# Kernel optimization log

Hardware: AMD Instinct MI355X
Metric: run time of the kernel (lower is better)

The kernel has to match this reference:

```python
import jax, jax.numpy as jnp
import numpy as np

BS, NS, NCP, NH, C, HID, R = 8, 2048, 8, 8, 128, 128, 128


def rotation_6d_to_matrix(d6):
    a1, a2 = d6[..., :3], d6[..., 3:]
    b1 = a1 / jnp.linalg.norm(a1, axis=-1, keepdims=True)
    b2 = a2 - jnp.sum(b1 * a2, axis=-1, keepdims=True) * b1
    b2 = b2 / jnp.linalg.norm(b2, axis=-1, keepdims=True)
    b3 = jnp.cross(b1, b2)
    return jnp.stack([b1, b2, b3], axis=-2)  # (..., 3, 3), rows b1,b2,b3


def _sample_plane(plane, uv):
    # plane: (B,C,R,R); uv: (B,N,2) in [0,1]; uv[...,0]->width, uv[...,1]->height
    Rr = plane.shape[-1]
    x = jnp.clip(uv[..., 0], 0.0, 1.0) * (Rr - 1)
    y = jnp.clip(uv[..., 1], 0.0, 1.0) * (Rr - 1)
    x0 = jnp.floor(x); y0 = jnp.floor(y)
    wx = x - x0; wy = y - y0
    x0i = x0.astype(jnp.int32); y0i = y0.astype(jnp.int32)
    x1i = jnp.minimum(x0i + 1, Rr - 1); y1i = jnp.minimum(y0i + 1, Rr - 1)
    gb = jax.vmap(lambda p, yi, xi: p[:, yi, xi])  # per-batch gather -> (C,N)
    f00 = gb(plane, y0i, x0i); f01 = gb(plane, y0i, x1i)
    f10 = gb(plane, y1i, x0i); f11 = gb(plane, y1i, x1i)
    wx = wx[:, None, :]; wy = wy[:, None, :]
    f = f00 * (1 - wx) * (1 - wy) + f01 * wx * (1 - wy) + f10 * (1 - wx) * wy + f11 * wx * wy
    return jnp.transpose(f, (0, 2, 1))  # (B,N,C)


def triplane_sample(p, pxz, pxy, pyz):
    # p: (B,N,3) in [0,1]^3; sum of bilinear samples from the three planes
    return (_sample_plane(pxz, p[..., jnp.array([0, 2])])
            + _sample_plane(pxy, p[..., jnp.array([0, 1])])
            + _sample_plane(pyz, p[..., jnp.array([1, 2])]))


def setup_inputs() -> dict:
    key = jax.random.key(0)
    ks = jax.random.split(key, 10)
    s = 1.0 / np.sqrt(C)
    return {
        "query_pos": jax.random.uniform(ks[0], (BS, NS, 9), dtype=jnp.float32),
        "plane_xz": jax.random.normal(ks[1], (BS, C, R, R), dtype=jnp.float32),
        "plane_xy": jax.random.normal(ks[2], (BS, C, R, R), dtype=jnp.float32),
        "plane_yz": jax.random.normal(ks[3], (BS, C, R, R), dtype=jnp.float32),
        "control_points": jax.random.normal(ks[4], (NCP, 3), dtype=jnp.float32) * 0.05,
        "W_v": jax.random.normal(ks[5], (C, HID), dtype=jnp.float32) * s,
        "b_v": jnp.zeros((HID,), jnp.float32),
        "W_w": jax.random.normal(ks[6], (C, NCP * NH), dtype=jnp.float32) * s,
        "b_w": jnp.zeros((NCP * NH,), jnp.float32),
        "W_o": jax.random.normal(ks[7], (HID, C), dtype=jnp.float32) * s,
        "b_o": jnp.zeros((C,), jnp.float32),
    }


def reference(query_pos, plane_xz, plane_xy, plane_yz, control_points,
              W_v, b_v, W_w, b_w, W_o, b_o):
    bs, ns, _ = query_pos.shape
    q_ori = query_pos[..., 3:]
    q_pos = query_pos[..., :3]
    feature = triplane_sample(q_pos, plane_xz, plane_xy, plane_yz)  # (bs,ns,C)
    rot = rotation_6d_to_matrix(q_ori)  # (bs,ns,3,3)
    # rotate control points: einsum('bnpd,bngd->bngp') with cp broadcast over (bs,ns)
    cp = jnp.einsum('bnpd,gd->bngp', rot, control_points)  # (bs,ns,ncp,3)
    anchor = q_pos[:, :, None, :] + cp  # (bs,ns,ncp,3)
    sf = triplane_sample(anchor.reshape(bs, ns * NCP, 3), plane_xz, plane_xy, plane_yz)
    sf = sf.reshape(bs * ns, NCP, C)  # head dim in torch code is a pure repeat
    feat = feature.reshape(bs * ns, C)
    w = (feat @ W_w + b_w).reshape(bs * ns, NCP, NH)  # (B,ncp,heads)
    vbase = sf @ W_v + b_v  # (B,ncp,hid); identical across repeated head dim
    # torch: (v * weights).sum((1,2)) with v_t[b,i,j,k]=vbase[b,j,k], w[b,i,j]
    out = jnp.einsum('bjk,bij->bk', vbase, w)  # (B,hid)
    out = out @ W_o + b_o
    out = out + feat
    return out.reshape(bs, ns, -1)
```

## Files before the change

### kernel.cpp

```cpp
#include <hip/hip_runtime.h>
#include <hip/hip_fp16.h>
#include <math.h>

constexpr int BS  = 8;
constexpr int NS  = 2048;
constexpr int NCP = 8;
constexpr int NH  = 8;
constexpr int C   = 128;
constexpr int HID = 128;
constexpr int RR  = 128;

constexpr int QPB = 8;
constexpr int VEC = 4;

constexpr size_t PLE = (size_t)BS * RR * RR * C;

struct F4 { float x, y, z, w; };
__device__ __forceinline__ F4 f4add(F4 a, F4 b) {
    return F4{a.x + b.x, a.y + b.y, a.z + b.z, a.w + b.w};
}
__device__ __forceinline__ F4 f4fma(F4 acc, float s, F4 v) {
    return F4{fmaf(s, v.x, acc.x), fmaf(s, v.y, acc.y),
              fmaf(s, v.z, acc.z), fmaf(s, v.w, acc.w)};
}
__device__ __forceinline__ F4 cvt4(int2 r) {
    __half2 h0 = *reinterpret_cast<__half2*>(&r.x);
    __half2 h1 = *reinterpret_cast<__half2*>(&r.y);
    float2 f0 = __half22float2(h0);
    float2 f1 = __half22float2(h1);
    return F4{f0.x, f0.y, f1.x, f1.y};
}

__global__ __launch_bounds__(256) void transpose_k(
    const float* __restrict__ pxz, const float* __restrict__ pxy,
    const float* __restrict__ pyz, __half* __restrict__ dst)
{
    const int z  = blockIdx.z;
    const int pl = z >> 3;
    const int b  = z & 7;
    const float* src = (pl == 0 ? pxz : (pl == 1 ? pxy : pyz)) + (size_t)b * C * RR * RR;
    __half* d = dst + (size_t)z * (RR * RR * C);

    __shared__ float tile[32][33];
    const int N  = RR * RR;
    const int n0 = blockIdx.x * 32;
    const int m0 = blockIdx.y * 32;
    const int tx = threadIdx.x, ty = threadIdx.y;

    #pragma unroll
    for (int ii = 0; ii < 4; ++ii)
        tile[ty + ii * 8][tx] = src[(size_t)(m0 + ty + ii * 8) * N + n0 + tx];
    __syncthreads();
    #pragma unroll
    for (int ii = 0; ii < 4; ++ii)
        d[(size_t)(n0 + ty + ii * 8) * C + m0 + tx] = __float2half(tile[tx][ty + ii * 8]);
}

__global__ __launch_bounds__(128) void prepw_k(
    const float* __restrict__ Wv, const float* __restrict__ bv,
    const float* __restrict__ Ww, const float* __restrict__ bw,
    const float* __restrict__ Wo,
    float* __restrict__ Wf, float* __restrict__ bf,
    float* __restrict__ Ww2, float* __restrict__ bw2)
{
    const int k = blockIdx.x, c = threadIdx.x;
    if (k < 128) {
        float acc = 0.f;
        #pragma unroll 8
        for (int j = 0; j < 128; ++j) acc += Wv[k * 128 + j] * Wo[j * 128 + c];
        Wf[k * 128 + c] = acc;
    } else if (k == 128) {
        float acc = 0.f;
        #pragma unroll 8
        for (int j = 0; j < 128; ++j) acc += bv[j] * Wo[j * 128 + c];
        bf[c] = acc;
    } else {
        float s[NH];
        #pragma unroll
        for (int h = 0; h < NH; ++h) s[h] = 0.f;
        #pragma unroll
        for (int i = 0; i < NCP; ++i)
            #pragma unroll
            for (int h = 0; h < NH; ++h) s[h] += Ww[c * (NCP * NH) + i * NH + h];
        #pragma unroll
        for (int h = 0; h < NH; ++h) Ww2[c * NH + h] = s[h];
        if (c < NH) {
            float t = 0.f;
            #pragma unroll
            for (int i = 0; i < NCP; ++i) t += bw[i * NH + c];
            bw2[c] = t;
        }
    }
}

__device__ __forceinline__ F4 samp(const __half* __restrict__ base, float u, float v)
{
    float x = fminf(fmaxf(u, 0.f), 1.f) * (float)(RR - 1);
    float y = fminf(fmaxf(v, 0.f), 1.f) * (float)(RR - 1);
    float x0f = floorf(x), y0f = floorf(y);
    float wx = x - x0f, wy = y - y0f;
    int x0 = (int)x0f, y0 = (int)y0f;
    int x1 = min(x0 + 1, RR - 1), y1 = min(y0 + 1, RR - 1);
    int r0 = y0 << 14, r1 = y1 << 14, cc0 = x0 << 7, cc1 = x1 << 7;
    int2 a00 = *reinterpret_cast<const int2*>(base + r0 + cc0);
    int2 a01 = *reinterpret_cast<const int2*>(base + r0 + cc1);
    int2 a10 = *reinterpret_cast<const int2*>(base + r1 + cc0);
    int2 a11 = *reinterpret_cast<const int2*>(base + r1 + cc1);
    float w00 = (1.f - wx) * (1.f - wy), w01 = wx * (1.f - wy);
    float w10 = (1.f - wx) * wy,         w11 = wx * wy;
    F4 f00 = cvt4(a00), f01 = cvt4(a01), f10 = cvt4(a10), f11 = cvt4(a11);
    F4 r;
    r.x = f00.x * w00 + f01.x * w01 + f10.x * w10 + f11.x * w11;
    r.y = f00.y * w00 + f01.y * w01 + f10.y * w10 + f11.y * w11;
    r.z = f00.z * w00 + f01.z * w01 + f10.z * w10 + f11.z * w11;
    r.w = f00.w * w00 + f01.w * w01 + f10.w * w10 + f11.w * w11;
    return r;
}

__global__ __launch_bounds__(256) void attn_k(
    const float* __restrict__ qpos,
    const __half* __restrict__ planes,
    const float* __restrict__ cpts,
    const float* __restrict__ Ww2, const float* __restrict__ bw2,
    const float* __restrict__ Wf,  const float* __restrict__ bf,
    const float* __restrict__ bo,
    float* __restrict__ out)
{
    const int nb   = gridDim.x;
    const int cpx  = nb >> 3;
    const int sbid = (blockIdx.x & 7) * cpx + (blockIdx.x >> 3);

    const int tid  = threadIdx.x;
    const int ql   = tid >> 5;
    const int lane = tid & 31;
    const int c4   = lane * VEC;
    const int q    = sbid * QPB + ql;
    const int b    = q >> 11;

    const float* qp = qpos + (size_t)q * 9;
    const float px = qp[0], py = qp[1], pz = qp[2];
    const float a1x = qp[3], a1y = qp[4], a1z = qp[5];
    const float a2x = qp[6], a2y = qp[7], a2z = qp[8];

    float inv = 1.f / sqrtf(a1x * a1x + a1y * a1y + a1z * a1z);
    float b1x = a1x * inv, b1y = a1y * inv, b1z = a1z * inv;
    float dd  = b1x * a2x + b1y * a2y + b1z * a2z;
    float b2x = a2x - dd * b1x, b2y = a2y - dd * b1y, b2z = a2z - dd * b1z;
    inv = 1.f / sqrtf(b2x * b2x + b2y * b2y + b2z * b2z);
    b2x *= inv; b2y *= inv; b2z *= inv;
    float b3x = b1y * b2z - b1z * b2y;
    float b3y = b1z * b2x - b1x * b2z;
    float b3z = b1x * b2y - b1y * b2x;

    const __half* Pxz = planes + (size_t)b * (RR * RR * C) + c4;
    const __half* Pxy = Pxz + PLE;
    const __half* Pyz = Pxy + PLE;

    F4 feat = f4add(f4add(samp(Pxz, px, pz), samp(Pxy, px, py)), samp(Pyz, py, pz));

    float p[NH];
    #pragma unroll
    for (int h = 0; h < NH; ++h) p[h] = 0.f;
    {
        const float* wr = Ww2 + c4 * NH;
        const float fv[VEC] = {feat.x, feat.y, feat.z, feat.w};
        #pragma unroll
        for (int i = 0; i < VEC; ++i)
            #pragma unroll
            for (int h = 0; h < NH; ++h) p[h] += fv[i] * wr[i * NH + h];
    }
    #pragma unroll
    for (int off = 16; off >= 1; off >>= 1)
        #pragma unroll
        for (int h = 0; h < NH; ++h) p[h] += __shfl_xor(p[h], off);

    float ws[NH], Ssum = 0.f;
    #pragma unroll
    for (int h = 0; h < NH; ++h) { ws[h] = p[h] + bw2[h]; Ssum += ws[h]; }

    F4 comb = {0.f, 0.f, 0.f, 0.f};
    #pragma unroll 2
    for (int g = 0; g < NCP; ++g) {
        float cx = cpts[g * 3 + 0], cy = cpts[g * 3 + 1], cz = cpts[g * 3 + 2];
        float ax = px + b1x * cx + b1y * cy + b1z * cz;
        float ay = py + b2x * cx + b2y * cy + b2z * cz;
        float az = pz + b3x * cx + b3y * cy + b3z * cz;
        F4 s = f4add(f4add(samp(Pxz, ax, az), samp(Pxy, ax, ay)), samp(Pyz, ay, az));
        comb = f4fma(comb, ws[g], s);
    }

    __shared__ float sComb[QPB][C];
    __shared__ float sFeat[QPB][C];
    __shared__ float sSum[QPB];
    *reinterpret_cast<float4*>(&sComb[ql][c4]) = make_float4(comb.x, comb.y, comb.z, comb.w);
    *reinterpret_cast<float4*>(&sFeat[ql][c4]) = make_float4(feat.x, feat.y, feat.z, feat.w);
    if (lane == 0) sSum[ql] = Ssum;
    __syncthreads();

    const int c  = tid & 127;
    const int q0 = (tid >> 7) * 4;
    float acc[4];
    const float bfc = bf[c], boc = bo[c];
    #pragma unroll
    for (int j = 0; j < 4; ++j)
        acc[j] = sSum[q0 + j] * bfc + boc + sFeat[q0 + j][c];
    #pragma unroll 4
    for (int k = 0; k < C; ++k) {
        float wf = Wf[k * C + c];
        #pragma unroll
        for (int j = 0; j < 4; ++j) acc[j] += sComb[q0 + j][k] * wf;
    }
    #pragma unroll
    for (int j = 0; j < 4; ++j)
        out[(size_t)(sbid * QPB + q0 + j) * C + c] = acc[j];
}

extern "C" void kernel_launch(void* const* d_in, const int* in_sizes, int n_in,
                              void* d_out, int out_size, void* d_ws, size_t ws_size,
                              hipStream_t stream)
{
    const float* qpos = (const float*)d_in[0];
    const float* pxz  = (const float*)d_in[1];
    const float* pxy  = (const float*)d_in[2];
    const float* pyz  = (const float*)d_in[3];
    const float* cpts = (const float*)d_in[4];
    const float* Wv   = (const float*)d_in[5];
    const float* bv   = (const float*)d_in[6];
    const float* Ww   = (const float*)d_in[7];
    const float* bw   = (const float*)d_in[8];
    const float* Wo   = (const float*)d_in[9];
    const float* bo   = (const float*)d_in[10];
    float* out = (float*)d_out;

    __half* plh = (__half*)d_ws;
    float*  wsf = (float*)((char*)d_ws + 3 * PLE * sizeof(__half));
    float* Wf  = wsf;
    float* bf  = Wf + C * HID;
    float* Ww2 = bf + C;
    float* bw2 = Ww2 + C * NH;

    {
        dim3 tb(32, 8, 1);
        dim3 tg(RR * RR / 32, C / 32, 3 * BS);
        hipLaunchKernelGGL(transpose_k, tg, tb, 0, stream, pxz, pxy, pyz, plh);
    }
    hipLaunchKernelGGL(prepw_k, dim3(130), dim3(128), 0, stream,
                       Wv, bv, Ww, bw, Wo, Wf, bf, Ww2, bw2);
    hipLaunchKernelGGL(attn_k, dim3(BS * NS / QPB), dim3(256), 0, stream,
                       qpos, plh, cpts, Ww2, bw2, Wf, bf, bo, out);
}
```

Before: 126.7 us.

## Fuse plane transpose with weight prep and widen transpose tiles

```diff
diff --git a/kernel.cpp b/kernel.cpp
--- a/kernel.cpp
+++ b/kernel.cpp
@@ -13,7 +13,12 @@
 constexpr int QPB = 8;
 constexpr int VEC = 4;
 
-constexpr size_t PLE = (size_t)BS * RR * RR * C;
+constexpr int NPOS = RR * RR;
+constexpr size_t PLE = (size_t)BS * NPOS * C;
+
+constexpr int TPOS   = 64;
+constexpr int NBLK_T = 3 * BS * (NPOS / TPOS);
+constexpr int LDSP   = 132;
 
 struct F4 { float x, y, z, w; };
 __device__ __forceinline__ F4 f4add(F4 a, F4 b) {
@@ -31,65 +36,83 @@
     return F4{f0.x, f0.y, f1.x, f1.y};
 }
 
-__global__ __launch_bounds__(256) void transpose_k(
+__global__ __launch_bounds__(256) void trans_prep_k(
     const float* __restrict__ pxz, const float* __restrict__ pxy,
-    const float* __restrict__ pyz, __half* __restrict__ dst)
-{
-    const int z  = blockIdx.z;
-    const int pl = z >> 3;
-    const int b  = z & 7;
-    const float* src = (pl == 0 ? pxz : (pl == 1 ? pxy : pyz)) + (size_t)b * C * RR * RR;
-    __half* d = dst + (size_t)z * (RR * RR * C);
-
-    __shared__ float tile[32][33];
-    const int N  = RR * RR;
-    const int n0 = blockIdx.x * 32;
-    const int m0 = blockIdx.y * 32;
-    const int tx = threadIdx.x, ty = threadIdx.y;
-
-    #pragma unroll
-    for (int ii = 0; ii < 4; ++ii)
-        tile[ty + ii * 8][tx] = src[(size_t)(m0 + ty + ii * 8) * N + n0 + tx];
-    __syncthreads();
-    #pragma unroll
-    for (int ii = 0; ii < 4; ++ii)
-        d[(size_t)(n0 + ty + ii * 8) * C + m0 + tx] = __float2half(tile[tx][ty + ii * 8]);
-}
-
-__global__ __launch_bounds__(128) void prepw_k(
+    const float* __restrict__ pyz, __half* __restrict__ dst,
     const float* __restrict__ Wv, const float* __restrict__ bv,
     const float* __restrict__ Ww, const float* __restrict__ bw,
     const float* __restrict__ Wo,
     float* __restrict__ Wf, float* __restrict__ bf,
     float* __restrict__ Ww2, float* __restrict__ bw2)
 {
-    const int k = blockIdx.x, c = threadIdx.x;
-    if (k < 128) {
-        float acc = 0.f;
-        #pragma unroll 8
-        for (int j = 0; j < 128; ++j) acc += Wv[k * 128 + j] * Wo[j * 128 + c];
-        Wf[k * 128 + c] = acc;
-    } else if (k == 128) {
-        float acc = 0.f;
-        #pragma unroll 8
-        for (int j = 0; j < 128; ++j) acc += bv[j] * Wo[j * 128 + c];
-        bf[c] = acc;
-    } else {
-        float s[NH];
-        #pragma unroll
-        for (int h = 0; h < NH; ++h) s[h] = 0.f;
-        #pragma unroll
-        for (int i = 0; i < NCP; ++i)
-            #pragma unroll
-            for (int h = 0; h < NH; ++h) s[h] += Ww[c * (NCP * NH) + i * NH + h];
-        #pragma unroll
-        for (int h = 0; h < NH; ++h) Ww2[c * NH + h] = s[h];
-        if (c < NH) {
-            float t = 0.f;
-            #pragma unroll
-            for (int i = 0; i < NCP; ++i) t += bw[i * NH + c];
-            bw2[c] = t;
+    const int bid = blockIdx.x;
+    const int t   = threadIdx.x;
+
+    if (bid >= NBLK_T) {
+        const int k = bid - NBLK_T;
+        const int c = t;
+        if (c >= 128) return;
+        if (k < 128) {
+            float acc = 0.f;
+            #pragma unroll 8
+            for (int j = 0; j < 128; ++j) acc += Wv[k * 128 + j] * Wo[j * 128 + c];
+            Wf[k * 128 + c] = acc;
+        } else if (k == 128) {
+            float acc = 0.f;
+            #pragma unroll 8
+            for (int j = 0; j < 128; ++j) acc += bv[j] * Wo[j * 128 + c];
+            bf[c] = acc;
+        } else {
+            float s[NH];
+            #pragma unroll
+            for (int h = 0; h < NH; ++h) s[h] = 0.f;
+            #pragma unroll
+            for (int i = 0; i < NCP; ++i)
+                #pragma unroll
+                for (int h = 0; h < NH; ++h) s[h] += Ww[c * (NCP * NH) + i * NH + h];
+            #pragma unroll
+            for (int h = 0; h < NH; ++h) Ww2[c * NH + h] = s[h];
+            if (c < NH) {
+                float tt = 0.f;
+                #pragma unroll
+                for (int i = 0; i < NCP; ++i) tt += bw[i * NH + c];
+                bw2[c] = tt;
+            }
         }
+        return;
+    }
+
+    const int b   = bid & 7;
+    const int idx = bid >> 3;
+    const int pl  = idx >> 8;
+    const int n0  = (idx & 255) * TPOS;
+
+    const float* src = (pl == 0 ? pxz : (pl == 1 ? pxy : pyz))
+                       + (size_t)b * C * NPOS;
+    __half* d = dst + (size_t)(pl * BS + b) * ((size_t)NPOS * C);
+
+    __shared__ __half lds[TPOS * LDSP];
+
+    #pragma unroll
+    for (int i = 0; i < 8; ++i) {
+        int li = i * 256 + t;
+        int m  = li >> 4;
+        int k4 = (li & 15) << 2;
+        float4 v = *reinterpret_cast<const float4*>(src + (size_t)m * NPOS + n0 + k4);
+        lds[(k4 + 0) * LDSP + m] = __float2half(v.x);
+        lds[(k4 + 1) * LDSP + m] = __float2half(v.y);
+        lds[(k4 + 2) * LDSP + m] = __float2half(v.z);
+        lds[(k4 + 3) * LDSP + m] = __float2half(v.w);
+    }
+    __syncthreads();
+
+    #pragma unroll
+    for (int i = 0; i < 8; ++i) {
+        int li = i * 256 + t;
+        int n  = li >> 5;
+        int c4 = (li & 31) << 2;
+        uint2 v = *reinterpret_cast<const uint2*>(lds + n * LDSP + c4);
+        *reinterpret_cast<uint2*>(d + (size_t)(n0 + n) * C + c4) = v;
     }
 }
 
@@ -152,7 +175,7 @@
     float b3y = b1z * b2x - b1x * b2z;
     float b3z = b1x * b2y - b1y * b2x;
 
-    const __half* Pxz = planes + (size_t)b * (RR * RR * C) + c4;
+    const __half* Pxz = planes + (size_t)b * ((size_t)NPOS * C) + c4;
     const __half* Pxy = Pxz + PLE;
     const __half* Pyz = Pxy + PLE;
 
@@ -239,13 +262,9 @@
     float* Ww2 = bf + C;
     float* bw2 = Ww2 + C * NH;
 
-    {
-        dim3 tb(32, 8, 1);
-        dim3 tg(RR * RR / 32, C / 32, 3 * BS);
-        hipLaunchKernelGGL(transpose_k, tg, tb, 0, stream, pxz, pxy, pyz, plh);
-    }
-    hipLaunchKernelGGL(prepw_k, dim3(130), dim3(128), 0, stream,
-                       Wv, bv, Ww, bw, Wo, Wf, bf, Ww2, bw2);
+    hipLaunchKernelGGL(trans_prep_k, dim3(NBLK_T + 130), dim3(256), 0, stream,
+                       pxz, pxy, pyz, plh, Wv, bv, Ww, bw, Wo, Wf, bf, Ww2, bw2);
+
     hipLaunchKernelGGL(attn_k, dim3(BS * NS / QPB), dim3(256), 0, stream,
                        qpos, plh, cpts, Ww2, bw2, Wf, bf, bo, out);
 }
```

Result: faster. 121.2 us (-4.3%).
